# Optimization experiments

Hardware: AMD Instinct MI355X
Metric: run time of the kernel (lower is better)

## Reference

```python
import jax, jax.numpy as jnp
import numpy as np

L, B, E, H, NL = 512, 8, 1024, 16, 2
HD = E // H
DFF = 4 * E
EPS = 1e-5


def setup_inputs() -> dict:
    key = jax.random.key(0)
    ks = jax.random.split(key, 8)
    s = 0.02
    return {
        "src": jax.random.normal(ks[0], (L, B, E), jnp.float32),
        "position_embed": jax.random.normal(ks[1], (L, L, HD), jnp.float32) * s,
        "type_embed": jax.random.normal(ks[2], (L, L, HD), jnp.float32) * s,
        "Wi": jax.random.normal(ks[3], (NL, 3 * E, E), jnp.float32) * s,
        "bi": jnp.zeros((NL, 3 * E), jnp.float32),
        "Wo": jax.random.normal(ks[4], (NL, E, E), jnp.float32) * s,
        "bo": jnp.zeros((NL, E), jnp.float32),
        "W1": jax.random.normal(ks[5], (NL, DFF, E), jnp.float32) * s,
        "b1": jnp.zeros((NL, DFF), jnp.float32),
        "W2": jax.random.normal(ks[6], (NL, E, DFF), jnp.float32) * s,
        "b2": jnp.zeros((NL, E), jnp.float32),
        "g1": jnp.ones((NL, E), jnp.float32),
        "be1": jnp.zeros((NL, E), jnp.float32),
        "g2": jnp.ones((NL, E), jnp.float32),
        "be2": jnp.zeros((NL, E), jnp.float32),
    }


def _ln(x, g, b):
    m = jnp.mean(x, -1, keepdims=True)
    v = jnp.mean((x - m) ** 2, -1, keepdims=True)
    return (x - m) * jax.lax.rsqrt(v + EPS) * g + b


def _attn(src, pos, typ, Wi, bi, Wo, bo):
    # src: [L, B, E]
    p = src @ Wi.T + bi                      # [L, B, 3E]
    q, k, v = jnp.split(p, 3, axis=-1)
    q = q * (HD ** -0.5)
    # -> [B, H, L, HD]
    def hsplit(t):
        return t.reshape(L, B, H, HD).transpose(1, 2, 0, 3)
    q, k, v = hsplit(q), hsplit(k), hsplit(v)
    # scores = q k^T + type_embed@q + q@pos^T  (Shaw relative attention)
    scores = jnp.einsum('bhld,bhsd->bhls', q, k)
    scores = scores + jnp.einsum('bhld,lsd->bhls', q, pos)      # position term
    scores = scores + jnp.einsum('lsd,bhld->bhls', typ, q)      # type term
    w = jax.nn.softmax(scores, axis=-1)                          # [B, H, L, S]
    # output = w v + w@pos + typ^T@w
    out = jnp.einsum('bhls,bhsd->bhld', w, v)
    out = out + jnp.einsum('bhls,lsd->bhld', w, pos)
    out = out + jnp.einsum('bhls,lsd->bhld', w, typ)
    out = out.transpose(2, 0, 1, 3).reshape(L, B, E)            # [L, B, E]
    return out @ Wo.T + bo


def _layer(src, pos, typ, Wi, bi, Wo, bo, W1, b1, W2, b2, g1, be1, g2, be2):
    src2 = _attn(src, pos, typ, Wi, bi, Wo, bo)
    src = _ln(src + src2, g1, be1)
    h = jax.nn.gelu(src @ W1.T + b1, approximate=False)
    src2 = h @ W2.T + b2
    return _ln(src + src2, g2, be2)


def reference(src, position_embed, type_embed, Wi, bi, Wo, bo, W1, b1, W2, b2,
              g1, be1, g2, be2):
    out = src
    for i in range(NL):
        out = _layer(out, position_embed, type_embed,
                     Wi[i], bi[i], Wo[i], bo[i], W1[i], b1[i], W2[i], b2[i],
                     g1[i], be1[i], g2[i], be2[i])
    return out
```

## Files before the change

### kernel.cpp

```cpp
#include <hip/hip_runtime.h>
#include <hip/hip_bf16.h>
#include <math.h>


typedef __hip_bfloat16 bf16;
typedef short short8 __attribute__((ext_vector_type(8)));
typedef float f32x4 __attribute__((ext_vector_type(4)));

constexpr int Lc = 512;
constexpr int Bc = 8;
constexpr int Ec = 1024;
constexpr int Hc = 16;
constexpr int HDc = 64;
constexpr int NLc = 2;
constexpr int DFFc = 4096;
constexpr int LB = Lc * Bc;
constexpr int BHc = Bc * Hc;
constexpr float EPSc = 1e-5f;

__device__ inline unsigned short f2bfu(float f) {
  union { __hip_bfloat16 h; unsigned short u; } cv;
  cv.h = __float2bfloat16(f);
  return cv.u;
}

template <bool ACC, bool GELU, bool OBF>
__global__ __launch_bounds__(256) void gemm_bt(
    int M, int N, int K,
    const bf16* __restrict__ A, int lda, long long sAz,
    const bf16* __restrict__ Bm, int ldb, long long sBz,
    void* __restrict__ Cv, int ldc, long long sCz,
    const float* __restrict__ bias) {
  __shared__ __align__(16) bf16 As[128 * 72];
  __shared__ __align__(16) bf16 Bs[64 * 72];
  const int tid = threadIdx.x;
  const int w = tid >> 6, lane = tid & 63, quad = lane >> 4, lr = lane & 15;
  const int m0 = blockIdx.x * 128, n0 = blockIdx.y * 64;
  const long long z = blockIdx.z;
  A += z * sAz;
  Bm += z * sBz;
  float* Cf = (float*)Cv;
  bf16* Cb = (bf16*)Cv;

  f32x4 acc[2][4];
#pragma unroll
  for (int i = 0; i < 2; i++)
#pragma unroll
    for (int j = 0; j < 4; j++) acc[i][j] = {0.f, 0.f, 0.f, 0.f};

  for (int k0 = 0; k0 < K; k0 += 64) {
#pragma unroll
    for (int i = 0; i < 8; i++) {
      int slot = tid + i * 256;
      int r = slot >> 4, c4 = (slot & 15) << 2;
      const bf16* srcp = A + (long long)(m0 + r) * lda + k0 + c4;
      *(ushort4*)&As[r * 72 + c4] = *(const ushort4*)srcp;
    }
#pragma unroll
    for (int i = 0; i < 4; i++) {
      int slot = tid + i * 256;
      int r = slot >> 4, c4 = (slot & 15) << 2;
      const bf16* srcp = Bm + (long long)(n0 + r) * ldb + k0 + c4;
      *(ushort4*)&Bs[r * 72 + c4] = *(const ushort4*)srcp;
    }
    __syncthreads();
#pragma unroll
    for (int ks = 0; ks < 64; ks += 32) {
      short8 a[2], b[4];
#pragma unroll
      for (int i = 0; i < 2; i++)
        a[i] = *(const short8*)&As[(w * 32 + i * 16 + lr) * 72 + ks + quad * 8];
#pragma unroll
      for (int j = 0; j < 4; j++)
        b[j] = *(const short8*)&Bs[(j * 16 + lr) * 72 + ks + quad * 8];
#pragma unroll
      for (int i = 0; i < 2; i++)
#pragma unroll
        for (int j = 0; j < 4; j++)
          acc[i][j] = __builtin_amdgcn_mfma_f32_16x16x32_bf16(a[i], b[j], acc[i][j], 0, 0, 0);
    }
    __syncthreads();
  }

#pragma unroll
  for (int i = 0; i < 2; i++) {
#pragma unroll
    for (int j = 0; j < 4; j++) {
      int col = n0 + j * 16 + lr;
      float bv = bias ? bias[col] : 0.f;
#pragma unroll
      for (int r = 0; r < 4; r++) {
        int row = m0 + w * 32 + i * 16 + quad * 4 + r;
        long long off = z * sCz + (long long)row * ldc + col;
        float v = acc[i][j][r] + bv;
        if (ACC) v += Cf[off];
        if (GELU) v = 0.5f * v * (1.f + erff(v * 0.70710678118654752f));
        if (OBF)
          Cb[off] = __float2bfloat16(v);
        else
          Cf[off] = v;
      }
    }
  }
}

__global__ void cvt_bf16(const float* __restrict__ in, bf16* __restrict__ out, long long n) {
  long long i = (long long)blockIdx.x * 256 + threadIdx.x;
  if (i < n) out[i] = __float2bfloat16(in[i]);
}

__global__ void init_x(const float* __restrict__ src, float* __restrict__ x, bf16* __restrict__ xb) {
  long long i = (long long)blockIdx.x * 256 + threadIdx.x;
  float v = src[i];
  x[i] = v;
  xb[i] = __float2bfloat16(v);
}

__global__ void prep_R(const float* __restrict__ pos, const float* __restrict__ typ,
                       bf16* __restrict__ Rb, bf16* __restrict__ Rt) {
  __shared__ __align__(16) float Ls[64 * 68];
  int l = blockIdx.y, s0 = blockIdx.x * 64;
  int tid = threadIdx.x;
#pragma unroll
  for (int i = 0; i < 4; i++) {
    int slot = tid + i * 256;
    int r = slot >> 4, c = (slot & 15) << 2;
    long long off = (((long long)l) * Lc + s0 + r) * HDc + c;
    float4 a = *(const float4*)&pos[off];
    float4 b = *(const float4*)&typ[off];
    float4 s = {a.x + b.x, a.y + b.y, a.z + b.z, a.w + b.w};
    *(float4*)&Ls[r * 68 + c] = s;
    ushort4 o = {f2bfu(s.x), f2bfu(s.y), f2bfu(s.z), f2bfu(s.w)};
    *(ushort4*)&Rb[off] = o;
  }
  __syncthreads();
#pragma unroll
  for (int i = 0; i < 4; i++) {
    int slot = tid + i * 256;
    int d = slot >> 4, s4 = (slot & 15) << 2;
    ushort4 o = {f2bfu(Ls[(s4 + 0) * 68 + d]), f2bfu(Ls[(s4 + 1) * 68 + d]),
                 f2bfu(Ls[(s4 + 2) * 68 + d]), f2bfu(Ls[(s4 + 3) * 68 + d])};
    *(ushort4*)&Rt[(((long long)l) * HDc + d) * Lc + s0 + s4] = o;
  }
}

__global__ void split_qk(const float* __restrict__ P, bf16* __restrict__ q, bf16* __restrict__ k) {
  long long idx = (long long)blockIdx.x * 256 + threadIdx.x;
  int col = idx & (Ec - 1);
  long long row = idx >> 10;
  int l = (int)(row >> 3), b = (int)(row & 7);
  int h = col >> 6, d = col & 63;
  long long dst = (((long long)(b * Hc + h)) * Lc + l) * HDc + d;
  q[dst] = __float2bfloat16(P[row * 3072 + col] * 0.125f);
  k[dst] = __float2bfloat16(P[row * 3072 + Ec + col]);
}

__global__ void transpose_v(const float* __restrict__ P, bf16* __restrict__ vt) {
  __shared__ __align__(16) float Ls[64 * 68];
  int bh = blockIdx.y, b = bh >> 4, h = bh & 15;
  int l0 = blockIdx.x * 64;
  int tid = threadIdx.x;
#pragma unroll
  for (int i = 0; i < 4; i++) {
    int slot = tid + i * 256;
    int r = slot >> 4, c = (slot & 15) << 2;
    float4 v = *(const float4*)&P[((long long)(l0 + r) * Bc + b) * 3072 + 2 * Ec + h * 64 + c];
    *(float4*)&Ls[r * 68 + c] = v;
  }
  __syncthreads();
#pragma unroll
  for (int i = 0; i < 4; i++) {
    int slot = tid + i * 256;
    int d = slot >> 4, s4 = (slot & 15) << 2;
    ushort4 o = {f2bfu(Ls[(s4 + 0) * 68 + d]), f2bfu(Ls[(s4 + 1) * 68 + d]),
                 f2bfu(Ls[(s4 + 2) * 68 + d]), f2bfu(Ls[(s4 + 3) * 68 + d])};
    *(ushort4*)&vt[(((long long)(b * Hc + h)) * HDc + d) * Lc + l0 + s4] = o;
  }
}

__global__ __launch_bounds__(256) void softmax_rows(const float* S, bf16* P) {
  int w = threadIdx.x >> 6, lane = threadIdx.x & 63;
  long long row = (long long)blockIdx.x * 4 + w;
  const float* sr = S + row * 512;
  float4 v0 = *(const float4*)(sr + lane * 4);
  float4 v1 = *(const float4*)(sr + 256 + lane * 4);
  float mx = fmaxf(fmaxf(fmaxf(v0.x, v0.y), fmaxf(v0.z, v0.w)),
                   fmaxf(fmaxf(v1.x, v1.y), fmaxf(v1.z, v1.w)));
#pragma unroll
  for (int o = 32; o; o >>= 1) mx = fmaxf(mx, __shfl_xor(mx, o, 64));
  float e[8];
  e[0] = __expf(v0.x - mx); e[1] = __expf(v0.y - mx);
  e[2] = __expf(v0.z - mx); e[3] = __expf(v0.w - mx);
  e[4] = __expf(v1.x - mx); e[5] = __expf(v1.y - mx);
  e[6] = __expf(v1.z - mx); e[7] = __expf(v1.w - mx);
  float sum = e[0] + e[1] + e[2] + e[3] + e[4] + e[5] + e[6] + e[7];
#pragma unroll
  for (int o = 32; o; o >>= 1) sum += __shfl_xor(sum, o, 64);
  float inv = 1.f / sum;
  ushort4 o0 = {f2bfu(e[0] * inv), f2bfu(e[1] * inv), f2bfu(e[2] * inv), f2bfu(e[3] * inv)};
  ushort4 o1 = {f2bfu(e[4] * inv), f2bfu(e[5] * inv), f2bfu(e[6] * inv), f2bfu(e[7] * inv)};
  *(ushort4*)(P + row * 1024 + lane * 4) = o0;
  *(ushort4*)(P + row * 1024 + 256 + lane * 4) = o1;
}

__global__ void merge_ao(const float* __restrict__ ao2, bf16* __restrict__ aob) {
  long long i = (long long)blockIdx.x * 256 + threadIdx.x;
  int d = (int)(i & 63);
  long long t = i >> 6;
  int l = (int)(t & (Lc - 1));
  long long bh = t >> 9;
  int b = (int)(bh >> 4), h = (int)(bh & 15);
  aob[((long long)(l * Bc + b)) * Ec + h * 64 + d] = __float2bfloat16(ao2[i]);
}

__global__ __launch_bounds__(256) void add_ln(const float* __restrict__ X, const float* __restrict__ Cin,
                                              const float* __restrict__ g, const float* __restrict__ be,
                                              float* __restrict__ outF, bf16* __restrict__ outB) {
  __shared__ float s_sum[4], s_sq[4];
  long long row = blockIdx.x;
  int tid = threadIdx.x;
  float4 xv = *(const float4*)&X[row * Ec + tid * 4];
  float4 cv = *(const float4*)&Cin[row * Ec + tid * 4];
  float v[4] = {xv.x + cv.x, xv.y + cv.y, xv.z + cv.z, xv.w + cv.w};
  float sm = v[0] + v[1] + v[2] + v[3];
  float sq = v[0] * v[0] + v[1] * v[1] + v[2] * v[2] + v[3] * v[3];
#pragma unroll
  for (int o = 32; o; o >>= 1) {
    sm += __shfl_xor(sm, o, 64);
    sq += __shfl_xor(sq, o, 64);
  }
  int w = tid >> 6, lane = tid & 63;
  if (lane == 0) {
    s_sum[w] = sm;
    s_sq[w] = sq;
  }
  __syncthreads();
  sm = s_sum[0] + s_sum[1] + s_sum[2] + s_sum[3];
  sq = s_sq[0] + s_sq[1] + s_sq[2] + s_sq[3];
  float mean = sm * (1.f / Ec);
  float var = sq * (1.f / Ec) - mean * mean;
  float rs = rsqrtf(var + EPSc);
#pragma unroll
  for (int e = 0; e < 4; e++) {
    int n = tid * 4 + e;
    float o = (v[e] - mean) * rs * g[n] + be[n];
    outF[row * Ec + n] = o;
    outB[row * Ec + n] = __float2bfloat16(o);
  }
}

static constexpr size_t WS_NEED = 327155712;

struct GlobalWs {
  void* p = nullptr;
  GlobalWs() {
    if (hipMalloc(&p, WS_NEED) != hipSuccess) p = nullptr;
  }
};
static GlobalWs g_ws;

extern "C" void kernel_launch(void* const* d_in, const int* in_sizes, int n_in,
                              void* d_out, int out_size, void* d_ws, size_t ws_size,
                              hipStream_t stream) {
  const float* src = (const float*)d_in[0];
  const float* pos = (const float*)d_in[1];
  const float* typ = (const float*)d_in[2];
  const float* Wi = (const float*)d_in[3];
  const float* bi = (const float*)d_in[4];
  const float* Wo = (const float*)d_in[5];
  const float* bo = (const float*)d_in[6];
  const float* W1 = (const float*)d_in[7];
  const float* b1 = (const float*)d_in[8];
  const float* W2 = (const float*)d_in[9];
  const float* b2 = (const float*)d_in[10];
  const float* g1 = (const float*)d_in[11];
  const float* be1 = (const float*)d_in[12];
  const float* g2 = (const float*)d_in[13];
  const float* be2 = (const float*)d_in[14];
  float* out = (float*)d_out;
  (void)in_sizes; (void)n_in; (void)out_size;

  char* wp = (ws_size >= WS_NEED) ? (char*)d_ws : (char*)g_ws.p;
  if (!wp) wp = (char*)d_ws;
  auto alloc = [&](size_t bytes) {
    char* r = wp;
    wp += (bytes + 255) & ~(size_t)255;
    return r;
  };

  char* U = alloc((size_t)BHc * Lc * Lc * 4);
  float* P = (float*)U;
  float* scores = (float*)U;
  bf16* probs = (bf16*)U;
  bf16* hb = (bf16*)U;

  float* x = (float*)alloc((size_t)LB * Ec * 4);
  bf16* xb = (bf16*)alloc((size_t)LB * Ec * 2);
  bf16* q = (bf16*)alloc((size_t)BHc * Lc * HDc * 2);
  bf16* k = (bf16*)alloc((size_t)BHc * Lc * HDc * 2);
  bf16* vt = (bf16*)alloc((size_t)BHc * HDc * Lc * 2);
  float* ao2 = (float*)alloc((size_t)BHc * Lc * HDc * 4);
  float* c1 = ao2;
  bf16* aob = (bf16*)alloc((size_t)LB * Ec * 2);
  bf16* Rb = (bf16*)alloc((size_t)Lc * Lc * HDc * 2);
  bf16* Rt = (bf16*)alloc((size_t)Lc * HDc * Lc * 2);
  bf16* wib = (bf16*)alloc((size_t)NLc * 3 * Ec * Ec * 2);
  bf16* wob = (bf16*)alloc((size_t)NLc * Ec * Ec * 2);
  bf16* w1b = (bf16*)alloc((size_t)NLc * DFFc * Ec * 2);
  bf16* w2b = (bf16*)alloc((size_t)NLc * Ec * DFFc * 2);

  {
    long long n;
    n = (long long)NLc * 3 * Ec * Ec;
    cvt_bf16<<<(int)((n + 255) / 256), 256, 0, stream>>>(Wi, wib, n);
    n = (long long)NLc * Ec * Ec;
    cvt_bf16<<<(int)((n + 255) / 256), 256, 0, stream>>>(Wo, wob, n);
    n = (long long)NLc * DFFc * Ec;
    cvt_bf16<<<(int)((n + 255) / 256), 256, 0, stream>>>(W1, w1b, n);
    n = (long long)NLc * Ec * DFFc;
    cvt_bf16<<<(int)((n + 255) / 256), 256, 0, stream>>>(W2, w2b, n);
  }
  prep_R<<<dim3(Lc / 64, Lc), 256, 0, stream>>>(pos, typ, Rb, Rt);
  init_x<<<LB * Ec / 256, 256, 0, stream>>>(src, x, xb);

  for (int i = 0; i < NLc; i++) {
    const bf16* Wi_b = wib + (size_t)i * 3 * Ec * Ec;
    const bf16* Wo_b = wob + (size_t)i * Ec * Ec;
    const bf16* W1_b = w1b + (size_t)i * DFFc * Ec;
    const bf16* W2_b = w2b + (size_t)i * Ec * DFFc;

    gemm_bt<false, false, false><<<dim3(LB / 128, 3 * Ec / 64, 1), 256, 0, stream>>>(
        LB, 3 * Ec, Ec, xb, Ec, 0, Wi_b, Ec, 0, P, 3 * Ec, 0, bi + (size_t)i * 3 * Ec);
    split_qk<<<LB * Ec / 256, 256, 0, stream>>>(P, q, k);
    transpose_v<<<dim3(Lc / 64, BHc), 256, 0, stream>>>(P, vt);

    gemm_bt<false, false, false><<<dim3(Lc / 128, Lc / 64, BHc), 256, 0, stream>>>(
        Lc, Lc, HDc, q, HDc, (long long)Lc * HDc, k, HDc, (long long)Lc * HDc,
        scores, Lc, (long long)Lc * Lc, nullptr);
    gemm_bt<true, false, false><<<dim3(1, Lc / 64, Lc), 256, 0, stream>>>(
        BHc, Lc, HDc, q, Lc * HDc, (long long)HDc, Rb, HDc, (long long)Lc * HDc,
        scores, Lc * Lc, (long long)Lc, nullptr);

    softmax_rows<<<BHc * Lc / 4, 256, 0, stream>>>(scores, probs);

    gemm_bt<false, false, false><<<dim3(Lc / 128, 1, BHc), 256, 0, stream>>>(
        Lc, HDc, Lc, probs, 1024, (long long)Lc * 1024, vt, Lc, (long long)HDc * Lc,
        ao2, HDc, (long long)Lc * HDc, nullptr);
    gemm_bt<true, false, false><<<dim3(1, 1, Lc), 256, 0, stream>>>(
        BHc, HDc, Lc, probs, Lc * 1024, (long long)1024, Rt, Lc, (long long)HDc * Lc,
        ao2, Lc * HDc, (long long)HDc, nullptr);

    merge_ao<<<BHc * Lc * HDc / 256, 256, 0, stream>>>(ao2, aob);

    gemm_bt<false, false, false><<<dim3(LB / 128, Ec / 64, 1), 256, 0, stream>>>(
        LB, Ec, Ec, aob, Ec, 0, Wo_b, Ec, 0, c1, Ec, 0, bo + (size_t)i * Ec);
    add_ln<<<LB, 256, 0, stream>>>(x, c1, g1 + (size_t)i * Ec, be1 + (size_t)i * Ec, x, xb);

    gemm_bt<false, true, true><<<dim3(LB / 128, DFFc / 64, 1), 256, 0, stream>>>(
        LB, DFFc, Ec, xb, Ec, 0, W1_b, Ec, 0, hb, DFFc, 0, b1 + (size_t)i * DFFc);
    gemm_bt<false, false, false><<<dim3(LB / 128, Ec / 64, 1), 256, 0, stream>>>(
        LB, Ec, DFFc, hb, DFFc, 0, W2_b, DFFc, 0, c1, Ec, 0, b2 + (size_t)i * Ec);

    float* outF = (i == NLc - 1) ? out : x;
    add_ln<<<LB, 256, 0, stream>>>(x, c1, g2 + (size_t)i * Ec, be2 + (size_t)i * Ec, outF, xb);
  }
}
```

Baseline: 1.219 ms.

## Add 128x128-tile GEMM with direct global-to-LDS loads and use it for most matmuls

Introduces a new bf16 MFMA GEMM kernel, gemm_bt128. Each block computes a 128x128 output tile with four waves, each owning a 64x64 sub-tile, and operand tiles are loaded straight into LDS with global_load_lds. This replaces the 128x64-tile kernel for the QKV, score, relative-position score, output-projection and FFN GEMMs, to raise data reuse per block and drop the register staging of loads. The LDS layout is unpadded with a 128-byte row stride, so the MFMA operand reads may hit bank conflicts. There is no double buffering, so loads and compute within a block stay serialized.

After: 1.323 ms. 8.5% more time.

```diff
diff --git a/kernel.cpp b/kernel.cpp
--- a/kernel.cpp
+++ b/kernel.cpp
@@ -6,6 +6,9 @@
 typedef __hip_bfloat16 bf16;
 typedef short short8 __attribute__((ext_vector_type(8)));
 typedef float f32x4 __attribute__((ext_vector_type(4)));
+
+typedef __attribute__((address_space(1))) const void gvoid;
+typedef __attribute__((address_space(3))) void lvoid;
 
 constexpr int Lc = 512;
 constexpr int Bc = 8;
@@ -22,6 +25,87 @@
   union { __hip_bfloat16 h; unsigned short u; } cv;
   cv.h = __float2bfloat16(f);
   return cv.u;
+}
+
+template <bool ACC, bool GELU, bool OBF>
+__global__ __launch_bounds__(256) void gemm_bt128(
+    int M, int N, int K,
+    const bf16* __restrict__ A, int lda, long long sAz,
+    const bf16* __restrict__ Bm, int ldb, long long sBz,
+    void* __restrict__ Cv, int ldc, long long sCz,
+    const float* __restrict__ bias) {
+  __shared__ __align__(16) bf16 As[128 * 64];
+  __shared__ __align__(16) bf16 Bs[128 * 64];
+  const int tid = threadIdx.x;
+  const int w = tid >> 6, lane = tid & 63, quad = lane >> 4, lr = lane & 15;
+  const int wr = w >> 1, wc = w & 1;
+  const int m0 = blockIdx.x * 128, n0 = blockIdx.y * 128;
+  const long long z = blockIdx.z;
+  A += z * sAz;
+  Bm += z * sBz;
+  float* Cf = (float*)Cv;
+  bf16* Cb = (bf16*)Cv;
+
+  f32x4 acc[4][4];
+#pragma unroll
+  for (int i = 0; i < 4; i++)
+#pragma unroll
+    for (int j = 0; j < 4; j++) acc[i][j] = {0.f, 0.f, 0.f, 0.f};
+
+  const int rA = lane >> 3;
+  const int cA = (lane & 7) * 8;
+
+  for (int k0 = 0; k0 < K; k0 += 64) {
+#pragma unroll
+    for (int t = 0; t < 4; ++t) {
+      const int chunk = w * 4 + t;
+      const int row = chunk * 8 + rA;
+      __builtin_amdgcn_global_load_lds(
+          (gvoid*)(A + (long long)(m0 + row) * lda + k0 + cA),
+          (lvoid*)(As + chunk * 512), 16, 0, 0);
+      __builtin_amdgcn_global_load_lds(
+          (gvoid*)(Bm + (long long)(n0 + row) * ldb + k0 + cA),
+          (lvoid*)(Bs + chunk * 512), 16, 0, 0);
+    }
+    __syncthreads();
+#pragma unroll
+    for (int ks = 0; ks < 64; ks += 32) {
+      short8 a[4], b[4];
+#pragma unroll
+      for (int i = 0; i < 4; i++)
+        a[i] = *(const short8*)&As[(wr * 64 + i * 16 + lr) * 64 + ks + quad * 8];
+#pragma unroll
+      for (int j = 0; j < 4; j++)
+        b[j] = *(const short8*)&Bs[(wc * 64 + j * 16 + lr) * 64 + ks + quad * 8];
+#pragma unroll
+      for (int i = 0; i < 4; i++)
+#pragma unroll
+        for (int j = 0; j < 4; j++)
+          acc[i][j] = __builtin_amdgcn_mfma_f32_16x16x32_bf16(a[i], b[j], acc[i][j], 0, 0, 0);
+    }
+    __syncthreads();
+  }
+
+#pragma unroll
+  for (int i = 0; i < 4; i++) {
+#pragma unroll
+    for (int j = 0; j < 4; j++) {
+      int col = n0 + wc * 64 + j * 16 + lr;
+      float bv = bias ? bias[col] : 0.f;
+#pragma unroll
+      for (int r = 0; r < 4; r++) {
+        int row = m0 + wr * 64 + i * 16 + quad * 4 + r;
+        long long off = z * sCz + (long long)row * ldc + col;
+        float v = acc[i][j][r] + bv;
+        if (ACC) v += Cf[off];
+        if (GELU) v = 0.5f * v * (1.f + erff(v * 0.70710678118654752f));
+        if (OBF)
+          Cb[off] = __float2bfloat16(v);
+        else
+          Cf[off] = v;
+      }
+    }
+  }
 }
 
 template <bool ACC, bool GELU, bool OBF>
@@ -329,15 +413,15 @@
     const bf16* W1_b = w1b + (size_t)i * DFFc * Ec;
     const bf16* W2_b = w2b + (size_t)i * Ec * DFFc;
 
-    gemm_bt<false, false, false><<<dim3(LB / 128, 3 * Ec / 64, 1), 256, 0, stream>>>(
+    gemm_bt128<false, false, false><<<dim3(LB / 128, 3 * Ec / 128, 1), 256, 0, stream>>>(
         LB, 3 * Ec, Ec, xb, Ec, 0, Wi_b, Ec, 0, P, 3 * Ec, 0, bi + (size_t)i * 3 * Ec);
     split_qk<<<LB * Ec / 256, 256, 0, stream>>>(P, q, k);
     transpose_v<<<dim3(Lc / 64, BHc), 256, 0, stream>>>(P, vt);
 
-    gemm_bt<false, false, false><<<dim3(Lc / 128, Lc / 64, BHc), 256, 0, stream>>>(
+    gemm_bt128<false, false, false><<<dim3(Lc / 128, Lc / 128, BHc), 256, 0, stream>>>(
         Lc, Lc, HDc, q, HDc, (long long)Lc * HDc, k, HDc, (long long)Lc * HDc,
         scores, Lc, (long long)Lc * Lc, nullptr);
-    gemm_bt<true, false, false><<<dim3(1, Lc / 64, Lc), 256, 0, stream>>>(
+    gemm_bt128<true, false, false><<<dim3(1, Lc / 128, Lc), 256, 0, stream>>>(
         BHc, Lc, HDc, q, Lc * HDc, (long long)HDc, Rb, HDc, (long long)Lc * HDc,
         scores, Lc * Lc, (long long)Lc, nullptr);
 
@@ -352,13 +436,13 @@
 
     merge_ao<<<BHc * Lc * HDc / 256, 256, 0, stream>>>(ao2, aob);
 
-    gemm_bt<false, false, false><<<dim3(LB / 128, Ec / 64, 1), 256, 0, stream>>>(
+    gemm_bt128<false, false, false><<<dim3(LB / 128, Ec / 128, 1), 256, 0, stream>>>(
         LB, Ec, Ec, aob, Ec, 0, Wo_b, Ec, 0, c1, Ec, 0, bo + (size_t)i * Ec);
     add_ln<<<LB, 256, 0, stream>>>(x, c1, g1 + (size_t)i * Ec, be1 + (size_t)i * Ec, x, xb);
 
-    gemm_bt<false, true, true><<<dim3(LB / 128, DFFc / 64, 1), 256, 0, stream>>>(
+    gemm_bt128<false, true, true><<<dim3(LB / 128, DFFc / 128, 1), 256, 0, stream>>>(
         LB, DFFc, Ec, xb, Ec, 0, W1_b, Ec, 0, hb, DFFc, 0, b1 + (size_t)i * DFFc);
-    gemm_bt<false, false, false><<<dim3(LB / 128, Ec / 64, 1), 256, 0, stream>>>(
+    gemm_bt128<false, false, false><<<dim3(LB / 128, Ec / 128, 1), 256, 0, stream>>>(
         LB, Ec, DFFc, hb, DFFc, 0, W2_b, DFFc, 0, c1, Ec, 0, b2 + (size_t)i * Ec);
 
     float* outF = (i == NLc - 1) ? out : x;
```
